# Optimization experiments

Measured on AMD Instinct MI355X. Metric: run time of the kernel, lower is better.

The kernel has to match this reference:

```python
import jax, jax.numpy as jnp
from jax import lax
import numpy as np

D = 128      # embedding_dim == GRU input_size == hidden_size
B, S, L = 256, 32, 32  # users, slates per user, slate length


def setup_inputs() -> dict:
    key = jax.random.key(0)
    ks = jax.random.split(key, 8)
    sc = 1.0 / np.sqrt(D)  # PyTorch GRU/Linear init scale
    return {
        "item_embs": jax.random.normal(ks[0], (B, S, L, D), jnp.float32),
        "user_embs": jax.random.normal(ks[1], (B, S, D), jnp.float32),
        "W_ih": jax.random.normal(ks[2], (3 * D, D), jnp.float32) * sc,
        "W_hh": jax.random.normal(ks[3], (3 * D, D), jnp.float32) * sc,
        "b_ih": jax.random.normal(ks[4], (3 * D,), jnp.float32) * sc,
        "b_hh": jax.random.normal(ks[5], (3 * D,), jnp.float32) * sc,
        "W_out": jax.random.normal(ks[6], (1, D), jnp.float32) * sc,
        "b_out": jax.random.normal(ks[7], (1,), jnp.float32) * sc,
    }


def reference(item_embs, user_embs, W_ih, W_hh, b_ih, b_hh, W_out, b_out):
    b, s, l, d = item_embs.shape
    x = item_embs.reshape(b * s, l, d)          # [N, L, D]
    h0 = user_embs.reshape(b * s, d)            # [N, D] initial hidden per slate

    # Precompute input-side gate projections for all timesteps (one big GEMM).
    gx = jnp.einsum('nld,gd->nlg', x, W_ih) + b_ih  # [N, L, 3D], PyTorch gate order r,z,n

    def step(h, gx_t):
        gh = h @ W_hh.T + b_hh                   # [N, 3D]
        xr, xz, xn = jnp.split(gx_t, 3, axis=-1)
        hr, hz, hn = jnp.split(gh, 3, axis=-1)
        r = jax.nn.sigmoid(xr + hr)
        z = jax.nn.sigmoid(xz + hz)
        n = jnp.tanh(xn + r * hn)
        h_new = (1.0 - z) * n + z * h
        return h_new, h_new

    _, hs = lax.scan(step, h0, jnp.swapaxes(gx, 0, 1))  # hs: [L, N, D]
    rnn_out = jnp.swapaxes(hs, 0, 1)             # [N, L, D]
    out = rnn_out @ W_out.T + b_out              # [N, L, 1]
    return out.reshape(b, s, l)
```

## Files before the change

kernel.cpp:

```cpp
#include <hip/hip_runtime.h>
#include <math.h>

#define DD   128
#define LL   32
#define MS   32
#define NT   1024
#define NSEQ 8192
#define XP   136
#define OLP  36

#define NFRAG      48
#define FRAGF      (NFRAG * 64 * 4)
#define SMEM_XH_X  (2 * FRAGF * 4)
#define SMEM_XH_H  (SMEM_XH_X + 2 * MS * XP * 2)
#define SMEM_OUTL  (SMEM_XH_H + 2 * MS * XP * 2)
#define SMEM_WOFL  (SMEM_OUTL + MS * OLP * 4)
#define SMEM_TOTAL (SMEM_WOFL + 4 * 64 * 8 * 2)

typedef short bf16x8 __attribute__((ext_vector_type(8)));
typedef float f32x4  __attribute__((ext_vector_type(4)));

#define MFMA __builtin_amdgcn_mfma_f32_16x16x32_bf16

__device__ __forceinline__ unsigned short f2bf(float f) {
    unsigned u = __float_as_uint(f);
    u += 0x7fffu + ((u >> 16) & 1u);
    return (unsigned short)(u >> 16);
}

#if __has_builtin(__builtin_amdgcn_cvt_pk_bf16_f32)
typedef __bf16 bf16x2_t __attribute__((ext_vector_type(2)));
__device__ __forceinline__ unsigned pack2(float a, float b) {
    union { bf16x2_t v; unsigned u; } c;
    c.v = __builtin_amdgcn_cvt_pk_bf16_f32(a, b);
    return c.u;
}
#else
__device__ __forceinline__ unsigned pack2(float a, float b) {
    return (unsigned)f2bf(a) | ((unsigned)f2bf(b) << 16);
}
#endif

__device__ __forceinline__ void pack8(float4 a, float4 b, unsigned short* dst) {
    union { unsigned u[4]; bf16x8 v; } pk;
    pk.u[0] = pack2(a.x, a.y); pk.u[1] = pack2(a.z, a.w);
    pk.u[2] = pack2(b.x, b.y); pk.u[3] = pack2(b.z, b.w);
    *(bf16x8*)dst = pk.v;
}

__device__ __forceinline__ float fast_rcp(float x) {
    return __builtin_amdgcn_rcpf(x);
}

__global__ void prep_weights(const float* __restrict__ Wih,
                             const float* __restrict__ Whh,
                             unsigned short* __restrict__ Wfrag) {
    int idx  = blockIdx.x * blockDim.x + threadIdx.x;
    int j    = idx & 7;
    int lane = (idx >> 3) & 63;
    int kk   = (idx >> 9) & 3;
    int sl   = (idx >> 11) & 7;
    int sg   = idx >> 14;
    int n = lane & 15, q = lane >> 4;
    int k  = kk * 32 + q * 8 + j;
    int g  = (sg >= 3) ? sg - 3 : sg;
    int gd = g * 128 + sl * 16 + n;
    const float* src = (sg >= 3) ? Whh : Wih;
    Wfrag[idx] = f2bf(src[gd * 128 + k]);
}

__global__ __launch_bounds__(NT, 4) void gru_mfma(
    const float* __restrict__ x,
    const float* __restrict__ h0,
    const unsigned short* __restrict__ Wfrag,
    const float* __restrict__ b_ih,
    const float* __restrict__ b_hh,
    const float* __restrict__ w_out,
    const float* __restrict__ b_out,
    float* __restrict__ out)
{
    extern __shared__ char smem[];
    float*          gxf  = (float*)(smem);
    unsigned short* xhx  = (unsigned short*)(smem + SMEM_XH_X);
    unsigned short* xhh  = (unsigned short*)(smem + SMEM_XH_H);
    float*          outl = (float*)(smem + SMEM_OUTL);
    unsigned short* wofl = (unsigned short*)(smem + SMEM_WOFL);

    const int tid  = threadIdx.x;
    const int n0   = blockIdx.x * MS;
    const int wv   = tid >> 6;
    const int lane = tid & 63;
    const int ln   = lane & 15;
    const int q    = lane >> 4;
    const bf16x8* W = (const bf16x8*)Wfrag;

    if (wv < 8) {
        const int d4 = wv * 16 + q * 4;
        const f32x4 bhn4 = *(const f32x4*)&b_hh[2*DD + d4];

        bf16x8 whr[4], whz[4], whn[4];
        #pragma unroll
        for (int kk = 0; kk < 4; ++kk) {
            whr[kk] = W[((24 + wv)*4 + kk)*64 + lane];
            whz[kk] = W[((32 + wv)*4 + kk)*64 + lane];
            whn[kk] = W[((40 + wv)*4 + kk)*64 + lane];
        }

        #pragma unroll
        for (int e = 0; e < 4; ++e) {
            int idx = tid * 4 + e;
            int j   = idx & 7;
            int l2  = (idx >> 3) & 63;
            int kk  = idx >> 9;
            int n2 = l2 & 15, q2 = l2 >> 4;
            wofl[idx] = (n2 == 0) ? f2bf(w_out[kk * 32 + q2 * 8 + j])
                                  : (unsigned short)0;
        }
        {
            const int gn = tid >> 4, gd8 = (tid & 15) * 8;
            const float* hb = h0 + (size_t)(n0 + gn) * DD + gd8;
            pack8(*(const float4*)hb, *(const float4*)(hb + 4),
                  &xhh[gn * XP + gd8]);
        }
        float4 hp0 = *(const float4*)&h0[(size_t)(n0 + ln) * DD + d4];
        float4 hp1 = *(const float4*)&h0[(size_t)(n0 + 16 + ln) * DD + d4];
        float hprev[8] = {hp0.x, hp0.y, hp0.z, hp0.w,
                          hp1.x, hp1.y, hp1.z, hp1.w};

        __syncthreads();
        __syncthreads();

        for (int t = 0; t < LL; ++t) {
            const int sl_ = t & 1;
            const float* gf = gxf + sl_ * FRAGF;
            f32x4 cr[2], cz[2], ch[2];
            #pragma unroll
            for (int st = 0; st < 2; ++st) {
                cr[st] = *(const f32x4*)&gf[(((0*8 + wv)*2 + st)*64 + lane)*4];
                cz[st] = *(const f32x4*)&gf[(((1*8 + wv)*2 + st)*64 + lane)*4];
                ch[st] = (f32x4){0.f, 0.f, 0.f, 0.f};
            }
            const unsigned short* hr0 = xhh + sl_*MS*XP + ln*XP;
            const unsigned short* hr1 = hr0 + 16*XP;
            __builtin_amdgcn_s_setprio(1);
            #pragma unroll
            for (int kk = 0; kk < 4; ++kk) {
                bf16x8 b0 = *(const bf16x8*)(hr0 + kk*32 + q*8);
                bf16x8 b1 = *(const bf16x8*)(hr1 + kk*32 + q*8);
                cr[0] = MFMA(whr[kk], b0, cr[0], 0,0,0);
                cr[1] = MFMA(whr[kk], b1, cr[1], 0,0,0);
                cz[0] = MFMA(whz[kk], b0, cz[0], 0,0,0);
                cz[1] = MFMA(whz[kk], b1, cz[1], 0,0,0);
                ch[0] = MFMA(whn[kk], b0, ch[0], 0,0,0);
                ch[1] = MFMA(whn[kk], b1, ch[1], 0,0,0);
            }
            __builtin_amdgcn_s_setprio(0);
            f32x4 gnx[2];
            #pragma unroll
            for (int st = 0; st < 2; ++st)
                gnx[st] = *(const f32x4*)&gf[(((2*8 + wv)*2 + st)*64 + lane)*4];

            unsigned short* hw = xhh + (sl_ ^ 1)*MS*XP;
            #pragma unroll
            for (int st = 0; st < 2; ++st) {
                float hh_[4];
                #pragma unroll
                for (int i = 0; i < 4; ++i) {
                    const float rr = fast_rcp(1.f + __expf(-cr[st][i]));
                    const float zz = fast_rcp(1.f + __expf(-cz[st][i]));
                    const float aa = gnx[st][i] + rr * (ch[st][i] + bhn4[i]);
                    const float ee = __expf(-2.f * aa);
                    const float th = 2.f * fast_rcp(1.f + ee) - 1.f;
                    const float hh = th + zz * (hprev[st*4+i] - th);
                    hprev[st*4+i] = hh;
                    hh_[i] = hh;
                }
                union { unsigned u[2]; unsigned long long ull; } hv;
                hv.u[0] = pack2(hh_[0], hh_[1]);
                hv.u[1] = pack2(hh_[2], hh_[3]);
                *(unsigned long long*)&hw[(st*16 + ln)*XP + d4] = hv.ull;
            }
            __syncthreads();
        }
        __syncthreads();

        if (tid < 256) {
            const int row = tid >> 3;
            const int t4  = (tid & 7) * 4;
            float4 v = *(const float4*)&outl[row * OLP + t4];
            *(float4*)(out + (size_t)(n0 + row) * LL + t4) = v;
        }
    } else {
        const int pv = wv - 8;
        const int d4 = pv * 16 + q * 4;
        f32x4 br4, bz4, bn4;
        {
            f32x4 a0 = *(const f32x4*)&b_ih[d4];
            f32x4 a1 = *(const f32x4*)&b_hh[d4];
            br4 = a0 + a1;
            a0 = *(const f32x4*)&b_ih[DD + d4];
            a1 = *(const f32x4*)&b_hh[DD + d4];
            bz4 = a0 + a1;
            bn4 = *(const f32x4*)&b_ih[2*DD + d4];
        }
        const float bo = b_out[0];

        bf16x8 wxr[4], wxz[4], wxn[4];
        #pragma unroll
        for (int kk = 0; kk < 4; ++kk) {
            wxr[kk] = W[((0  + pv)*4 + kk)*64 + lane];
            wxz[kk] = W[((8  + pv)*4 + kk)*64 + lane];
            wxn[kk] = W[((16 + pv)*4 + kk)*64 + lane];
        }

        const int pt  = tid & 511;
        const int gn  = pt >> 4;
        const int gd8 = (pt & 15) * 8;
        const float* xbase = x + ((size_t)(n0 + gn) * LL) * DD + gd8;

        pack8(*(const float4*)(xbase), *(const float4*)(xbase + 4),
              &xhx[gn * XP + gd8]);
        pack8(*(const float4*)(xbase + DD), *(const float4*)(xbase + DD + 4),
              &xhx[MS*XP + gn * XP + gd8]);

        __syncthreads();

#define GX_STEP(TT)                                                            \
        {                                                                      \
            const int sr = (TT) & 1;                                           \
            const unsigned short* xr0 = xhx + sr*MS*XP + ln*XP;                \
            const unsigned short* xr1 = xr0 + 16*XP;                           \
            f32x4 ar[2], az[2], an[2];                                         \
            ar[0] = br4; ar[1] = br4;                                          \
            az[0] = bz4; az[1] = bz4;                                          \
            an[0] = bn4; an[1] = bn4;                                          \
            _Pragma("unroll")                                                  \
            for (int kk = 0; kk < 4; ++kk) {                                   \
                bf16x8 b0 = *(const bf16x8*)(xr0 + kk*32 + q*8);               \
                bf16x8 b1 = *(const bf16x8*)(xr1 + kk*32 + q*8);               \
                ar[0] = MFMA(wxr[kk], b0, ar[0], 0,0,0);                       \
                ar[1] = MFMA(wxr[kk], b1, ar[1], 0,0,0);                       \
                az[0] = MFMA(wxz[kk], b0, az[0], 0,0,0);                       \
                az[1] = MFMA(wxz[kk], b1, az[1], 0,0,0);                       \
                an[0] = MFMA(wxn[kk], b0, an[0], 0,0,0);                       \
                an[1] = MFMA(wxn[kk], b1, an[1], 0,0,0);                       \
            }                                                                  \
            float* gw = gxf + sr * FRAGF;                                      \
            _Pragma("unroll")                                                  \
            for (int st = 0; st < 2; ++st) {                                   \
                *(f32x4*)&gw[(((0*8 + pv)*2 + st)*64 + lane)*4] = ar[st];      \
                *(f32x4*)&gw[(((1*8 + pv)*2 + st)*64 + lane)*4] = az[st];      \
                *(f32x4*)&gw[(((2*8 + pv)*2 + st)*64 + lane)*4] = an[st];      \
            }                                                                  \
        }

        GX_STEP(0)
        __syncthreads();

        for (int t = 0; t < LL; ++t) {
            float4 sa, sb;
            const int ts = t + 2;
            if (ts < LL) {
                sa = *(const float4*)(xbase + (size_t)ts * DD);
                sb = *(const float4*)(xbase + (size_t)ts * DD + 4);
            }
            if (t + 1 < LL) GX_STEP(t + 1)

            if (pv < 2 && t >= 1) {
                f32x4 c4 = (f32x4){bo, bo, bo, bo};
                const unsigned short* hrw = xhh + (t & 1)*MS*XP + (pv*16 + ln)*XP;
                #pragma unroll
                for (int kk = 0; kk < 4; ++kk) {
                    bf16x8 a = *(const bf16x8*)&wofl[(kk*64 + lane)*8];
                    bf16x8 b = *(const bf16x8*)(hrw + kk*32 + q*8);
                    c4 = MFMA(a, b, c4, 0,0,0);
                }
                if (q == 0)
                    outl[(pv*16 + ln)*OLP + (t - 1)] = c4[0];
            }
            if (ts < LL)
                pack8(sa, sb, &xhx[(t & 1)*MS*XP + gn * XP + gd8]);

            __syncthreads();
        }

        if (pv < 2) {
            f32x4 c4 = (f32x4){bo, bo, bo, bo};
            const unsigned short* hrw = xhh + (pv*16 + ln)*XP;
            #pragma unroll
            for (int kk = 0; kk < 4; ++kk) {
                bf16x8 a = *(const bf16x8*)&wofl[(kk*64 + lane)*8];
                bf16x8 b = *(const bf16x8*)(hrw + kk*32 + q*8);
                c4 = MFMA(a, b, c4, 0,0,0);
            }
            if (q == 0)
                outl[(pv*16 + ln)*OLP + (LL - 1)] = c4[0];
        }
        __syncthreads();
#undef GX_STEP
    }
}

extern "C" void kernel_launch(void* const* d_in, const int* in_sizes, int n_in,
                              void* d_out, int out_size, void* d_ws, size_t ws_size,
                              hipStream_t stream) {
    const float* item  = (const float*)d_in[0];
    const float* user  = (const float*)d_in[1];
    const float* W_ih  = (const float*)d_in[2];
    const float* W_hh  = (const float*)d_in[3];
    const float* b_ih  = (const float*)d_in[4];
    const float* b_hh  = (const float*)d_in[5];
    const float* W_out = (const float*)d_in[6];
    const float* b_out = (const float*)d_in[7];
    float* out = (float*)d_out;

    unsigned short* Wfrag = (unsigned short*)d_ws;

    static bool smem_cfg = false;
    if (!smem_cfg) {
        hipFuncSetAttribute((const void*)gru_mfma,
                            hipFuncAttributeMaxDynamicSharedMemorySize,
                            SMEM_TOTAL);
        smem_cfg = true;
    }

    prep_weights<<<384, 256, 0, stream>>>(W_ih, W_hh, Wfrag);
    gru_mfma<<<NSEQ / MS, NT, SMEM_TOTAL, stream>>>(item, user, Wfrag,
                                                    b_ih, b_hh, W_out, b_out, out);
}
```

Measured before the change: 219.6 us.

## Halve sequences per block to 16 to double grid size

Each block now handles 16 sequences instead of 32. The per-wave MFMA work drops from two 16-column subtiles to one, shared memory shrinks, and the launch bound hint rises to 8. The b_hn bias is now folded into the accumulator init. This doubles the grid to spread the serial recurrence across more CUs and shortens each timestep's critical path. The cost is that W_hh/W_ih fragments are loaded into registers twice as many times overall and each MFMA does less reuse.

Result: slower. 461.4 us (+110.1%).

```diff
diff --git a/kernel.cpp b/kernel.cpp
--- a/kernel.cpp
+++ b/kernel.cpp
@@ -3,13 +3,13 @@
 
 #define DD   128
 #define LL   32
-#define MS   32
+#define MS   16
 #define NT   1024
 #define NSEQ 8192
 #define XP   136
 #define OLP  36
 
-#define NFRAG      48
+#define NFRAG      24
 #define FRAGF      (NFRAG * 64 * 4)
 #define SMEM_XH_X  (2 * FRAGF * 4)
 #define SMEM_XH_H  (SMEM_XH_X + 2 * MS * XP * 2)
@@ -41,11 +41,11 @@
 }
 #endif
 
-__device__ __forceinline__ void pack8(float4 a, float4 b, unsigned short* dst) {
-    union { unsigned u[4]; bf16x8 v; } pk;
-    pk.u[0] = pack2(a.x, a.y); pk.u[1] = pack2(a.z, a.w);
-    pk.u[2] = pack2(b.x, b.y); pk.u[3] = pack2(b.z, b.w);
-    *(bf16x8*)dst = pk.v;
+__device__ __forceinline__ void pack4(float4 a, unsigned short* dst) {
+    union { unsigned u[2]; unsigned long long ull; } pk;
+    pk.u[0] = pack2(a.x, a.y);
+    pk.u[1] = pack2(a.z, a.w);
+    *(unsigned long long*)dst = pk.ull;
 }
 
 __device__ __forceinline__ float fast_rcp(float x) {
@@ -69,7 +69,7 @@
     Wfrag[idx] = f2bf(src[gd * 128 + k]);
 }
 
-__global__ __launch_bounds__(NT, 4) void gru_mfma(
+__global__ __launch_bounds__(NT, 8) void gru_mfma(
     const float* __restrict__ x,
     const float* __restrict__ h0,
     const unsigned short* __restrict__ Wfrag,
@@ -117,15 +117,12 @@
                                   : (unsigned short)0;
         }
         {
-            const int gn = tid >> 4, gd8 = (tid & 15) * 8;
-            const float* hb = h0 + (size_t)(n0 + gn) * DD + gd8;
-            pack8(*(const float4*)hb, *(const float4*)(hb + 4),
-                  &xhh[gn * XP + gd8]);
-        }
-        float4 hp0 = *(const float4*)&h0[(size_t)(n0 + ln) * DD + d4];
-        float4 hp1 = *(const float4*)&h0[(size_t)(n0 + 16 + ln) * DD + d4];
-        float hprev[8] = {hp0.x, hp0.y, hp0.z, hp0.w,
-                          hp1.x, hp1.y, hp1.z, hp1.w};
+            const int gn = tid >> 5, gd4 = (tid & 31) * 4;
+            pack4(*(const float4*)&h0[(size_t)(n0 + gn) * DD + gd4],
+                  &xhh[gn * XP + gd4]);
+        }
+        float4 hp = *(const float4*)&h0[(size_t)(n0 + ln) * DD + d4];
+        float hprev[4] = {hp.x, hp.y, hp.z, hp.w};
 
         __syncthreads();
         __syncthreads();
@@ -133,58 +130,43 @@
         for (int t = 0; t < LL; ++t) {
             const int sl_ = t & 1;
             const float* gf = gxf + sl_ * FRAGF;
-            f32x4 cr[2], cz[2], ch[2];
-            #pragma unroll
-            for (int st = 0; st < 2; ++st) {
-                cr[st] = *(const f32x4*)&gf[(((0*8 + wv)*2 + st)*64 + lane)*4];
-                cz[st] = *(const f32x4*)&gf[(((1*8 + wv)*2 + st)*64 + lane)*4];
-                ch[st] = (f32x4){0.f, 0.f, 0.f, 0.f};
-            }
+            f32x4 cr = *(const f32x4*)&gf[((     wv)*64 + lane)*4];
+            f32x4 cz = *(const f32x4*)&gf[(( 8 + wv)*64 + lane)*4];
+            f32x4 ch = bhn4;
             const unsigned short* hr0 = xhh + sl_*MS*XP + ln*XP;
-            const unsigned short* hr1 = hr0 + 16*XP;
             __builtin_amdgcn_s_setprio(1);
             #pragma unroll
             for (int kk = 0; kk < 4; ++kk) {
                 bf16x8 b0 = *(const bf16x8*)(hr0 + kk*32 + q*8);
-                bf16x8 b1 = *(const bf16x8*)(hr1 + kk*32 + q*8);
-                cr[0] = MFMA(whr[kk], b0, cr[0], 0,0,0);
-                cr[1] = MFMA(whr[kk], b1, cr[1], 0,0,0);
-                cz[0] = MFMA(whz[kk], b0, cz[0], 0,0,0);
-                cz[1] = MFMA(whz[kk], b1, cz[1], 0,0,0);
-                ch[0] = MFMA(whn[kk], b0, ch[0], 0,0,0);
-                ch[1] = MFMA(whn[kk], b1, ch[1], 0,0,0);
+                cr = MFMA(whr[kk], b0, cr, 0,0,0);
+                cz = MFMA(whz[kk], b0, cz, 0,0,0);
+                ch = MFMA(whn[kk], b0, ch, 0,0,0);
             }
             __builtin_amdgcn_s_setprio(0);
-            f32x4 gnx[2];
+            f32x4 gnx = *(const f32x4*)&gf[((16 + wv)*64 + lane)*4];
+
+            unsigned short* hw = xhh + (sl_ ^ 1)*MS*XP;
+            float hh_[4];
             #pragma unroll
-            for (int st = 0; st < 2; ++st)
-                gnx[st] = *(const f32x4*)&gf[(((2*8 + wv)*2 + st)*64 + lane)*4];
-
-            unsigned short* hw = xhh + (sl_ ^ 1)*MS*XP;
-            #pragma unroll
-            for (int st = 0; st < 2; ++st) {
-                float hh_[4];
-                #pragma unroll
-                for (int i = 0; i < 4; ++i) {
-                    const float rr = fast_rcp(1.f + __expf(-cr[st][i]));
-                    const float zz = fast_rcp(1.f + __expf(-cz[st][i]));
-                    const float aa = gnx[st][i] + rr * (ch[st][i] + bhn4[i]);
-                    const float ee = __expf(-2.f * aa);
-                    const float th = 2.f * fast_rcp(1.f + ee) - 1.f;
-                    const float hh = th + zz * (hprev[st*4+i] - th);
-                    hprev[st*4+i] = hh;
-                    hh_[i] = hh;
-                }
-                union { unsigned u[2]; unsigned long long ull; } hv;
-                hv.u[0] = pack2(hh_[0], hh_[1]);
-                hv.u[1] = pack2(hh_[2], hh_[3]);
-                *(unsigned long long*)&hw[(st*16 + ln)*XP + d4] = hv.ull;
-            }
+            for (int i = 0; i < 4; ++i) {
+                const float rr = fast_rcp(1.f + __expf(-cr[i]));
+                const float zz = fast_rcp(1.f + __expf(-cz[i]));
+                const float aa = gnx[i] + rr * ch[i];
+                const float ee = __expf(-2.f * aa);
+                const float th = 2.f * fast_rcp(1.f + ee) - 1.f;
+                const float hh = th + zz * (hprev[i] - th);
+                hprev[i] = hh;
+                hh_[i] = hh;
+            }
+            union { unsigned u[2]; unsigned long long ull; } hv;
+            hv.u[0] = pack2(hh_[0], hh_[1]);
+            hv.u[1] = pack2(hh_[2], hh_[3]);
+            *(unsigned long long*)&hw[ln*XP + d4] = hv.ull;
             __syncthreads();
         }
         __syncthreads();
 
-        if (tid < 256) {
+        if (tid < 128) {
             const int row = tid >> 3;
             const int t4  = (tid & 7) * 4;
             float4 v = *(const float4*)&outl[row * OLP + t4];
@@ -214,14 +196,12 @@
         }
 
         const int pt  = tid & 511;
-        const int gn  = pt >> 4;
-        const int gd8 = (pt & 15) * 8;
-        const float* xbase = x + ((size_t)(n0 + gn) * LL) * DD + gd8;
-
-        pack8(*(const float4*)(xbase), *(const float4*)(xbase + 4),
-              &xhx[gn * XP + gd8]);
-        pack8(*(const float4*)(xbase + DD), *(const float4*)(xbase + DD + 4),
-              &xhx[MS*XP + gn * XP + gd8]);
+        const int gn  = pt >> 5;
+        const int gd4 = (pt & 31) * 4;
+        const float* xbase = x + ((size_t)(n0 + gn) * LL) * DD + gd4;
+
+        pack4(*(const float4*)(xbase),      &xhx[gn * XP + gd4]);
+        pack4(*(const float4*)(xbase + DD), &xhx[MS*XP + gn * XP + gd4]);
 
         __syncthreads();
 
@@ -229,46 +209,33 @@
         {                                                                      \
             const int sr = (TT) & 1;                                           \
             const unsigned short* xr0 = xhx + sr*MS*XP + ln*XP;                \
-            const unsigned short* xr1 = xr0 + 16*XP;                           \
-            f32x4 ar[2], az[2], an[2];                                         \
-            ar[0] = br4; ar[1] = br4;                                          \
-            az[0] = bz4; az[1] = bz4;                                          \
-            an[0] = bn4; an[1] = bn4;                                          \
+            f32x4 ar = br4, az = bz4, an = bn4;                                \
             _Pragma("unroll")                                                  \
             for (int kk = 0; kk < 4; ++kk) {                                   \
                 bf16x8 b0 = *(const bf16x8*)(xr0 + kk*32 + q*8);               \
-                bf16x8 b1 = *(const bf16x8*)(xr1 + kk*32 + q*8);               \
-                ar[0] = MFMA(wxr[kk], b0, ar[0], 0,0,0);                       \
-                ar[1] = MFMA(wxr[kk], b1, ar[1], 0,0,0);                       \
-                az[0] = MFMA(wxz[kk], b0, az[0], 0,0,0);                       \
-                az[1] = MFMA(wxz[kk], b1, az[1], 0,0,0);                       \
-                an[0] = MFMA(wxn[kk], b0, an[0], 0,0,0);                       \
-                an[1] = MFMA(wxn[kk], b1, an[1], 0,0,0);                       \
+                ar = MFMA(wxr[kk], b0, ar, 0,0,0);                             \
+                az = MFMA(wxz[kk], b0, az, 0,0,0);                             \
+                an = MFMA(wxn[kk], b0, an, 0,0,0);                             \
             }                                                                  \
             float* gw = gxf + sr * FRAGF;                                      \
-            _Pragma("unroll")                                                  \
-            for (int st = 0; st < 2; ++st) {                                   \
-                *(f32x4*)&gw[(((0*8 + pv)*2 + st)*64 + lane)*4] = ar[st];      \
-                *(f32x4*)&gw[(((1*8 + pv)*2 + st)*64 + lane)*4] = az[st];      \
-                *(f32x4*)&gw[(((2*8 + pv)*2 + st)*64 + lane)*4] = an[st];      \
-            }                                                                  \
+            *(f32x4*)&gw[((     pv)*64 + lane)*4] = ar;                        \
+            *(f32x4*)&gw[(( 8 + pv)*64 + lane)*4] = az;                        \
+            *(f32x4*)&gw[((16 + pv)*64 + lane)*4] = an;                        \
         }
 
         GX_STEP(0)
         __syncthreads();
 
         for (int t = 0; t < LL; ++t) {
-            float4 sa, sb;
+            float4 sa;
             const int ts = t + 2;
-            if (ts < LL) {
+            if (ts < LL)
                 sa = *(const float4*)(xbase + (size_t)ts * DD);
-                sb = *(const float4*)(xbase + (size_t)ts * DD + 4);
-            }
             if (t + 1 < LL) GX_STEP(t + 1)
 
-            if (pv < 2 && t >= 1) {
+            if (pv == 0 && t >= 1) {
                 f32x4 c4 = (f32x4){bo, bo, bo, bo};
-                const unsigned short* hrw = xhh + (t & 1)*MS*XP + (pv*16 + ln)*XP;
+                const unsigned short* hrw = xhh + (t & 1)*MS*XP + ln*XP;
                 #pragma unroll
                 for (int kk = 0; kk < 4; ++kk) {
                     bf16x8 a = *(const bf16x8*)&wofl[(kk*64 + lane)*8];
@@ -276,17 +243,17 @@
                     c4 = MFMA(a, b, c4, 0,0,0);
                 }
                 if (q == 0)
-                    outl[(pv*16 + ln)*OLP + (t - 1)] = c4[0];
+                    outl[ln*OLP + (t - 1)] = c4[0];
             }
             if (ts < LL)
-                pack8(sa, sb, &xhx[(t & 1)*MS*XP + gn * XP + gd8]);
+                pack4(sa, &xhx[(t & 1)*MS*XP + gn * XP + gd4]);
 
             __syncthreads();
         }
 
-        if (pv < 2) {
+        if (pv == 0) {
             f32x4 c4 = (f32x4){bo, bo, bo, bo};
-            const unsigned short* hrw = xhh + (pv*16 + ln)*XP;
+            const unsigned short* hrw = xhh + ln*XP;
             #pragma unroll
             for (int kk = 0; kk < 4; ++kk) {
                 bf16x8 a = *(const bf16x8*)&wofl[(kk*64 + lane)*8];
@@ -294,7 +261,7 @@
                 c4 = MFMA(a, b, c4, 0,0,0);
             }
             if (q == 0)
-                outl[(pv*16 + ln)*OLP + (LL - 1)] = c4[0];
+                outl[ln*OLP + (LL - 1)] = c4[0];
         }
         __syncthreads();
 #undef GX_STEP
```

## Move output projection into recurrence warps and merge sigmoid reciprocals

Applied to the files above, without the earlier changes.

The W_out projection MFMAs move from the producer (gate-projection) warps into recurrence warps 0-1, where they reuse the h fragments already loaded for the W_hh MFMAs. This takes work off the producer critical path and rebalances the two warp groups. The two sigmoid reciprocals are also fused into a single reciprocal of the product, with a clamp to avoid overflow. The b_hn bias is folded into the MFMA accumulator init. The catch is extra MFMA and LDS work on the latency-critical recurrence warps.

New measurement: 232.5 us. 1.06x slower.

```diff
diff --git a/kernel.cpp b/kernel.cpp
--- a/kernel.cpp
+++ b/kernel.cpp
@@ -97,6 +97,7 @@
     if (wv < 8) {
         const int d4 = wv * 16 + q * 4;
         const f32x4 bhn4 = *(const f32x4*)&b_hh[2*DD + d4];
+        const float bo   = b_out[0];
 
         bf16x8 whr[4], whz[4], whn[4];
         #pragma unroll
@@ -138,10 +139,11 @@
             for (int st = 0; st < 2; ++st) {
                 cr[st] = *(const f32x4*)&gf[(((0*8 + wv)*2 + st)*64 + lane)*4];
                 cz[st] = *(const f32x4*)&gf[(((1*8 + wv)*2 + st)*64 + lane)*4];
-                ch[st] = (f32x4){0.f, 0.f, 0.f, 0.f};
+                ch[st] = bhn4;
             }
             const unsigned short* hr0 = xhh + sl_*MS*XP + ln*XP;
             const unsigned short* hr1 = hr0 + 16*XP;
+            f32x4 c4 = (f32x4){bo, bo, bo, bo};
             __builtin_amdgcn_s_setprio(1);
             #pragma unroll
             for (int kk = 0; kk < 4; ++kk) {
@@ -153,8 +155,14 @@
                 cz[1] = MFMA(whz[kk], b1, cz[1], 0,0,0);
                 ch[0] = MFMA(whn[kk], b0, ch[0], 0,0,0);
                 ch[1] = MFMA(whn[kk], b1, ch[1], 0,0,0);
+                if (wv < 2) {
+                    bf16x8 a = *(const bf16x8*)&wofl[(kk*64 + lane)*8];
+                    c4 = MFMA(a, (wv == 0) ? b0 : b1, c4, 0,0,0);
+                }
             }
             __builtin_amdgcn_s_setprio(0);
+            if (wv < 2 && t >= 1 && q == 0)
+                outl[(wv*16 + ln)*OLP + (t - 1)] = c4[0];
             f32x4 gnx[2];
             #pragma unroll
             for (int st = 0; st < 2; ++st)
@@ -166,12 +174,16 @@
                 float hh_[4];
                 #pragma unroll
                 for (int i = 0; i < 4; ++i) {
-                    const float rr = fast_rcp(1.f + __expf(-cr[st][i]));
-                    const float zz = fast_rcp(1.f + __expf(-cz[st][i]));
-                    const float aa = gnx[st][i] + rr * (ch[st][i] + bhn4[i]);
+                    const float e1 = fminf(__expf(-cr[st][i]), 1e18f);
+                    const float e2 = fminf(__expf(-cz[st][i]), 1e18f);
+                    const float p1 = 1.f + e1, p2 = 1.f + e2;
+                    const float R  = fast_rcp(p1 * p2);
+                    const float rr = R * p2;
+                    const float zz = R * p1;
+                    const float aa = __builtin_fmaf(rr, ch[st][i], gnx[st][i]);
                     const float ee = __expf(-2.f * aa);
                     const float th = 2.f * fast_rcp(1.f + ee) - 1.f;
-                    const float hh = th + zz * (hprev[st*4+i] - th);
+                    const float hh = __builtin_fmaf(zz, hprev[st*4+i] - th, th);
                     hprev[st*4+i] = hh;
                     hh_[i] = hh;
                 }
@@ -181,6 +193,19 @@
                 *(unsigned long long*)&hw[(st*16 + ln)*XP + d4] = hv.ull;
             }
             __syncthreads();
+        }
+
+        if (wv < 2) {
+            f32x4 c4 = (f32x4){bo, bo, bo, bo};
+            const unsigned short* hrw = xhh + (wv*16 + ln)*XP;
+            #pragma unroll
+            for (int kk = 0; kk < 4; ++kk) {
+                bf16x8 a = *(const bf16x8*)&wofl[(kk*64 + lane)*8];
+                bf16x8 b = *(const bf16x8*)(hrw + kk*32 + q*8);
+                c4 = MFMA(a, b, c4, 0,0,0);
+            }
+            if (q == 0)
+                outl[(wv*16 + ln)*OLP + (LL - 1)] = c4[0];
         }
         __syncthreads();
 
@@ -203,7 +228,6 @@
             bz4 = a0 + a1;
             bn4 = *(const f32x4*)&b_ih[2*DD + d4];
         }
-        const float bo = b_out[0];
 
         bf16x8 wxr[4], wxz[4], wxn[4];
         #pragma unroll
@@ -266,35 +290,10 @@
             }
             if (t + 1 < LL) GX_STEP(t + 1)
 
-            if (pv < 2 && t >= 1) {
-                f32x4 c4 = (f32x4){bo, bo, bo, bo};
-                const unsigned short* hrw = xhh + (t & 1)*MS*XP + (pv*16 + ln)*XP;
-                #pragma unroll
-                for (int kk = 0; kk < 4; ++kk) {
-                    bf16x8 a = *(const bf16x8*)&wofl[(kk*64 + lane)*8];
-                    bf16x8 b = *(const bf16x8*)(hrw + kk*32 + q*8);
-                    c4 = MFMA(a, b, c4, 0,0,0);
-                }
-                if (q == 0)
-                    outl[(pv*16 + ln)*OLP + (t - 1)] = c4[0];
-            }
             if (ts < LL)
                 pack8(sa, sb, &xhx[(t & 1)*MS*XP + gn * XP + gd8]);
 
             __syncthreads();
-        }
-
-        if (pv < 2) {
-            f32x4 c4 = (f32x4){bo, bo, bo, bo};
-            const unsigned short* hrw = xhh + (pv*16 + ln)*XP;
-            #pragma unroll
-            for (int kk = 0; kk < 4; ++kk) {
-                bf16x8 a = *(const bf16x8*)&wofl[(kk*64 + lane)*8];
-                bf16x8 b = *(const bf16x8*)(hrw + kk*32 + q*8);
-                c4 = MFMA(a, b, c4, 0,0,0);
-            }
-            if (q == 0)
-                outl[(pv*16 + ln)*OLP + (LL - 1)] = c4[0];
         }
         __syncthreads();
 #undef GX_STEP
```
